# Kernel optimization log

Hardware: AMD Instinct MI355X
Metric: run time of the kernel (lower is better)

The kernel has to match this reference:

```python
import jax, jax.numpy as jnp
import numpy as np

EPS = 1e-6
SEARCH_RANGE = 4  # K = 2*R+1 = 9


def setup_inputs() -> dict:
    key = jax.random.key(0)
    k1, k2, k3, k4 = jax.random.split(key, 4)
    B, C, H, W = 4, 128, 128, 240
    E = 64
    F_L = jax.random.normal(k1, (B, C, H, W), dtype=jnp.float32)
    F_R = jax.random.normal(k2, (B, C, H, W), dtype=jnp.float32)
    d0 = jax.random.uniform(k3, (B, 1, H, W), dtype=jnp.float32) * 64.0  # pixel disparity
    phi_w = jax.random.normal(k4, (E, C), dtype=jnp.float32) / np.sqrt(C)  # 1x1 conv weight
    return {"F_L": F_L, "F_R": F_R, "d0": d0, "phi_w": phi_w}


def _embed(x, phi_w):
    # 1x1 conv + channel L2 normalize (cosine embedding)
    y = jnp.einsum('ec,bchw->behw', phi_w, x)
    norm = jnp.sqrt(jnp.sum(y * y, axis=1, keepdims=True)) + EPS
    return y / norm


def reference(F_L, F_R, d0, phi_w):
    R = SEARCH_RANGE
    FL = _embed(F_L, phi_w)  # (B,E,H,W)
    FR = _embed(F_R, phi_w)
    B, E, H, W = FL.shape
    deltas = jnp.arange(-R, R + 1, dtype=FL.dtype)  # (K,)
    xx = jnp.arange(W, dtype=FL.dtype)  # base x grid
    # x' = x - (d0 + delta); align_corners=True grid round-trips to pixel coords exactly,
    # y coordinate is identity, so warp is 1D bilinear along W with border clamp.
    xprime = xx[None, None, None, :] - d0[:, None, 0, :, :] - deltas[None, :, None, None]  # (B,K,H,W)
    x0 = jnp.floor(xprime)
    w = xprime - x0  # bilinear weight
    i0 = jnp.clip(x0.astype(jnp.int32), 0, W - 1)
    i1 = jnp.clip(x0.astype(jnp.int32) + 1, 0, W - 1)
    FR_e = FR[:, None]  # (B,1,E,H,W)
    g0 = jnp.take_along_axis(FR_e, i0[:, :, None, :, :], axis=4)  # (B,K,E,H,W)
    g1 = jnp.take_along_axis(FR_e, i1[:, :, None, :, :], axis=4)
    FR_s = g0 * (1.0 - w)[:, :, None] + g1 * w[:, :, None]
    cost_vol = jnp.einsum('behw,bkehw->bkhw', FL, FR_s)  # (B,K,H,W)
    return cost_vol
```

## Files before the change

### kernel.cpp

```cpp
#include <hip/hip_runtime.h>
#include <hip/hip_bf16.h>

#define NB 4
#define NC 128
#define NH 128
#define NW 240
#define NE 64
#define NK 9
#define PLANE (NH*NW)
#define CHW (NC*PLANE)
#define XS 244

typedef __attribute__((ext_vector_type(8))) short short8;
typedef __attribute__((ext_vector_type(4))) float f32x4;
typedef __attribute__((ext_vector_type(2))) __fp16 fp16x2;
typedef __attribute__((ext_vector_type(8))) __fp16 fp16x8;

__device__ __forceinline__ unsigned pkh(float x, float y){
  fp16x2 h = __builtin_amdgcn_cvt_pkrtz(x, y);
  return __builtin_bit_cast(unsigned, h);
}
__device__ __forceinline__ float fdot2u(unsigned a, unsigned b, float c){
#if __has_builtin(__builtin_amdgcn_fdot2)
  return __builtin_amdgcn_fdot2(__builtin_bit_cast(fp16x2,a),
                                __builtin_bit_cast(fp16x2,b), c, false);
#else
  fp16x2 ha = __builtin_bit_cast(fp16x2,a), hb = __builtin_bit_cast(fp16x2,b);
  return c + (float)ha[0]*(float)hb[0] + (float)ha[1]*(float)hb[1];
#endif
}
__device__ __forceinline__ int swz(int r){ return (r ^ (r>>3)) & 7; }

__global__ __launch_bounds__(1024, 8)
void fused_kernel(const float* __restrict__ xL,
                  const float* __restrict__ xR,
                  const float* __restrict__ d0g,
                  const float* __restrict__ phig,
                  float* __restrict__ outg)
{
  __shared__ __attribute__((aligned(16))) unsigned short xs[64*XS];
  __shared__ __attribute__((aligned(16))) unsigned short phis[NE*136];
  __shared__ __attribute__((aligned(16))) unsigned short FLb[NW*64];

  const int tid  = threadIdx.x;
  const int lane = tid & 63;
  const int wv   = tid >> 6;
  const int b    = blockIdx.x >> 7;
  const int h    = blockIdx.x & 127;
  const size_t base = (size_t)b*CHW + (size_t)h*NW;
  const int pixbase = (b*NH + h)*NW;

  const int mrow = lane & 15;
  const int kg   = lane >> 4;
  const int nt   = wv;
  const int n    = 16*nt + mrow;

  float d0v = (tid < 960) ? d0g[pixbase + (tid >> 2)] : 0.f;

  auto load_chunk = [&](const float* __restrict__ xg, int ch, float4 (&r)[4]) {
    if (tid < 960) {
      #pragma unroll
      for (int i = 0; i < 4; ++i) {
        unsigned idx = i*960 + tid;
        unsigned c = idx / 60u, s = idx - 60u*c;
        r[i] = *(const float4*)(xg + base + (size_t)(64*ch + c)*PLANE + 4*s);
      }
    }
  };
  auto write_chunk = [&](float4 (&r)[4]) {
    if (tid < 960) {
      #pragma unroll
      for (int i = 0; i < 4; ++i) {
        unsigned idx = i*960 + tid;
        unsigned c = idx / 60u, s = idx - 60u*c;
        uint2 pk; pk.x = pkh(r[i].x, r[i].y); pk.y = pkh(r[i].z, r[i].w);
        *(uint2*)&xs[c*XS + 4*s] = pk;
      }
    }
  };
  auto gemm_chunk = [&](f32x4 (&acc)[4], int ch) {
    if (nt < 15) {
      #pragma unroll
      for (int ks = 0; ks < 2; ++ks) {
        const int r0 = 32*ks + 8*kg;
        fp16x8 bv;
        #pragma unroll
        for (int j = 0; j < 8; ++j)
          bv[j] = *(const __fp16*)&xs[(r0 + j)*XS + n];
        #pragma unroll
        for (int mt = 0; mt < 4; ++mt) {
          short8 raw = *(const short8*)&phis[(16*mt + mrow)*136 + 64*ch + 32*ks + 8*kg];
          fp16x8 af = __builtin_bit_cast(fp16x8, raw);
          acc[mt] = __builtin_amdgcn_mfma_f32_16x16x32_f16(af, bv, acc[mt], 0, 0, 0);
        }
      }
    }
  };
  auto norm_pack = [&](f32x4 (&acc)[4], uint2 (&pk)[4]) {
    float ss = 0.f;
    #pragma unroll
    for (int mt = 0; mt < 4; ++mt)
      #pragma unroll
      for (int r = 0; r < 4; ++r)
        ss += acc[mt][r]*acc[mt][r];
    ss += __shfl_xor(ss, 16, 64);
    ss += __shfl_xor(ss, 32, 64);
    float inv = 1.f/(sqrtf(ss) + 1e-6f);
    #pragma unroll
    for (int mt = 0; mt < 4; ++mt) {
      pk[mt].x = pkh(acc[mt][0]*inv, acc[mt][1]*inv);
      pk[mt].y = pkh(acc[mt][2]*inv, acc[mt][3]*inv);
    }
  };

  float4 st[4];
  load_chunk(xL, 0, st);
  float4 pr[2];
  #pragma unroll
  for (int i = 0; i < 2; ++i) {
    int idx = i*1024 + tid;
    pr[i] = *(const float4*)(phig + (idx>>5)*128 + 4*(idx&31));
  }
  #pragma unroll
  for (int i = 0; i < 2; ++i) {
    int idx = i*1024 + tid;
    uint2 pk; pk.x = pkh(pr[i].x, pr[i].y); pk.y = pkh(pr[i].z, pr[i].w);
    *(uint2*)&phis[(idx>>5)*136 + 4*(idx&31)] = pk;
  }
  write_chunk(st);
  __syncthreads();

  f32x4 accL[4];
  #pragma unroll
  for (int mt = 0; mt < 4; ++mt) accL[mt] = (f32x4){0.f,0.f,0.f,0.f};

  load_chunk(xL, 1, st);
  gemm_chunk(accL, 0);
  __syncthreads();
  write_chunk(st);
  __syncthreads();

  load_chunk(xR, 0, st);
  gemm_chunk(accL, 1);
  uint2 flpk[4];
  norm_pack(accL, flpk);
  if (nt < 15) {
    #pragma unroll
    for (int mt = 0; mt < 4; ++mt) {
      int e0 = 16*mt + 4*kg;
      int pos = n*64 + (((e0>>3) ^ swz(n))<<3) + (e0&7);
      *(uint2*)&FLb[pos] = flpk[mt];
    }
  }
  __syncthreads();
  write_chunk(st);
  __syncthreads();

  f32x4 accR[4];
  #pragma unroll
  for (int mt = 0; mt < 4; ++mt) accR[mt] = (f32x4){0.f,0.f,0.f,0.f};

  load_chunk(xR, 1, st);
  gemm_chunk(accR, 0);
  __syncthreads();
  write_chunk(st);
  __syncthreads();

  gemm_chunk(accR, 1);
  uint2 frpk[4];
  norm_pack(accR, frpk);
  __syncthreads();

  unsigned short* FRb = &xs[0];
  if (nt < 15) {
    #pragma unroll
    for (int mt = 0; mt < 4; ++mt) {
      int e0 = 16*mt + 4*kg;
      int pos = n*64 + (((e0>>3) ^ swz(n))<<3) + (e0&7);
      *(uint2*)&FRb[pos] = frpk[mt];
    }
  }
  __syncthreads();

  float* cvb = (float*)phis;
  if (tid < 960) {
    const int p  = tid >> 2;
    const int eh = tid & 3;
    float xf  = (float)p - d0v;
    float x0  = floorf(xf);
    float wfr = xf - x0;
    int jb = (int)x0 - 4;

    unsigned fl[8];
    #pragma unroll
    for (int i = 0; i < 2; ++i) {
      int c4 = 2*eh + i;
      uint4 raw = *(const uint4*)&FLb[p*64 + ((c4 ^ swz(p))<<3)];
      fl[4*i+0]=raw.x; fl[4*i+1]=raw.y; fl[4*i+2]=raw.z; fl[4*i+3]=raw.w;
    }

    float D[10];
    #pragma unroll
    for (int t = 0; t < 10; ++t) {
      int j = jb + t;
      j = j < 0 ? 0 : (j > NW-1 ? NW-1 : j);
      float s = 0.f;
      #pragma unroll
      for (int i = 0; i < 2; ++i) {
        int c4 = 2*eh + i;
        uint4 raw = *(const uint4*)&FRb[j*64 + ((c4 ^ swz(j))<<3)];
        s = fdot2u(fl[4*i+0], raw.x, s);
        s = fdot2u(fl[4*i+1], raw.y, s);
        s = fdot2u(fl[4*i+2], raw.z, s);
        s = fdot2u(fl[4*i+3], raw.w, s);
      }
      D[t] = s;
    }
    #pragma unroll
    for (int t = 0; t < 10; ++t) {
      D[t] += __shfl_xor(D[t], 1, 64);
      D[t] += __shfl_xor(D[t], 2, 64);
    }

    #define WK(k) { const int t0 = 8-(k); cvb[(k)*NW + p] = (1.f - wfr)*D[t0] + wfr*D[t0+1]; }
    if      (eh == 0) { WK(0) WK(1) WK(2) }
    else if (eh == 1) { WK(3) WK(4) }
    else if (eh == 2) { WK(5) WK(6) }
    else              { WK(7) WK(8) }
    #undef WK
  }
  __syncthreads();

  if (tid < 540) {
    int k = tid/60, w4 = tid - 60*k;
    float4 v = *(const float4*)&cvb[k*NW + 4*w4];
    *(float4*)(outg + (size_t)b*NK*PLANE + (size_t)h*NW + (size_t)k*PLANE + 4*w4) = v;
  }
}

extern "C" void kernel_launch(void* const* d_in, const int* in_sizes, int n_in,
                              void* d_out, int out_size, void* d_ws, size_t ws_size,
                              hipStream_t stream) {
  const float* xL   = (const float*)d_in[0];
  const float* xR   = (const float*)d_in[1];
  const float* d0g  = (const float*)d_in[2];
  const float* phig = (const float*)d_in[3];
  float* outg = (float*)d_out;
  fused_kernel<<<dim3(NB*NH), dim3(1024), 0, stream>>>(xL, xR, d0g, phig, outg);
}
```

Baseline: 148.1 us.

## Stream input chunks directly to LDS with double-buffered global_load_lds pipeline

Replaces register-staged loads, fp16 conversion and LDS writes with direct global-to-LDS async loads (global_load_lds) into two fp32 LDS buffers of 32 channels each. Chunk loads are issued one stage ahead of the MFMA GEMM rounds, so memory traffic overlaps with compute. The fp16 conversion moves into the GEMM operand fetch. The separate FL buffer is dropped and the staging buffers are reused for the embeddings. This adds per-read conversions and relies on __syncthreads waiting for the outstanding LDS-direct loads.

```diff
diff --git a/kernel.cpp b/kernel.cpp
--- a/kernel.cpp
+++ b/kernel.cpp
@@ -9,7 +9,6 @@
 #define NK 9
 #define PLANE (NH*NW)
 #define CHW (NC*PLANE)
-#define XS 244
 
 typedef __attribute__((ext_vector_type(8))) short short8;
 typedef __attribute__((ext_vector_type(4))) float f32x4;
@@ -31,6 +30,16 @@
 }
 __device__ __forceinline__ int swz(int r){ return (r ^ (r>>3)) & 7; }
 
+__device__ __forceinline__ void gload_lds16(const float* g, float* lds_u, int lane){
+#if __has_builtin(__builtin_amdgcn_global_load_lds)
+  __builtin_amdgcn_global_load_lds(
+      (const __attribute__((address_space(1))) unsigned*)g,
+      (__attribute__((address_space(3))) unsigned*)lds_u, 16, 0, 0);
+#else
+  *(float4*)(lds_u + 4*lane) = *(const float4*)g;
+#endif
+}
+
 __global__ __launch_bounds__(1024, 8)
 void fused_kernel(const float* __restrict__ xL,
                   const float* __restrict__ xR,
@@ -38,9 +47,9 @@
                   const float* __restrict__ phig,
                   float* __restrict__ outg)
 {
-  __shared__ __attribute__((aligned(16))) unsigned short xs[64*XS];
+  __shared__ __attribute__((aligned(16))) float xs0[7680];
+  __shared__ __attribute__((aligned(16))) float xs1[7680];
   __shared__ __attribute__((aligned(16))) unsigned short phis[NE*136];
-  __shared__ __attribute__((aligned(16))) unsigned short FLb[NW*64];
 
   const int tid  = threadIdx.x;
   const int lane = tid & 63;
@@ -55,48 +64,38 @@
   const int nt   = wv;
   const int n    = 16*nt + mrow;
 
-  float d0v = (tid < 960) ? d0g[pixbase + (tid >> 2)] : 0.f;
-
-  auto load_chunk = [&](const float* __restrict__ xg, int ch, float4 (&r)[4]) {
-    if (tid < 960) {
-      #pragma unroll
-      for (int i = 0; i < 4; ++i) {
-        unsigned idx = i*960 + tid;
-        unsigned c = idx / 60u, s = idx - 60u*c;
-        r[i] = *(const float4*)(xg + base + (size_t)(64*ch + c)*PLANE + 4*s);
+  auto issue_chunk = [&](int q){
+    const float* src = (q < 4) ? xL : xR;
+    const int cb = 32*(q & 3);
+    float* buf = (q & 1) ? xs1 : xs0;
+    #pragma unroll
+    for (int i = 0; i < 2; ++i) {
+      int qq = 2*wv + i;
+      if (qq < 30) {
+        int g4 = qq*64 + lane;
+        int c = g4/60, s4 = g4 - 60*c;
+        gload_lds16(src + base + (size_t)(cb + c)*PLANE + 4*s4,
+                    buf + qq*256, lane);
       }
     }
   };
-  auto write_chunk = [&](float4 (&r)[4]) {
-    if (tid < 960) {
-      #pragma unroll
-      for (int i = 0; i < 4; ++i) {
-        unsigned idx = i*960 + tid;
-        unsigned c = idx / 60u, s = idx - 60u*c;
-        uint2 pk; pk.x = pkh(r[i].x, r[i].y); pk.y = pkh(r[i].z, r[i].w);
-        *(uint2*)&xs[c*XS + 4*s] = pk;
+
+  auto gemm_round = [&](const float* bf, int cb, f32x4 (&acc)[4]){
+    if (nt < 15) {
+      fp16x8 bv;
+      #pragma unroll
+      for (int j = 0; j < 8; ++j)
+        bv[j] = (__fp16)bf[(8*kg + j)*240 + n];
+      #pragma unroll
+      for (int mt = 0; mt < 4; ++mt) {
+        short8 raw = *(const short8*)&phis[(16*mt + mrow)*136 + cb + 8*kg];
+        fp16x8 af = __builtin_bit_cast(fp16x8, raw);
+        acc[mt] = __builtin_amdgcn_mfma_f32_16x16x32_f16(af, bv, acc[mt], 0, 0, 0);
       }
     }
   };
-  auto gemm_chunk = [&](f32x4 (&acc)[4], int ch) {
-    if (nt < 15) {
-      #pragma unroll
-      for (int ks = 0; ks < 2; ++ks) {
-        const int r0 = 32*ks + 8*kg;
-        fp16x8 bv;
-        #pragma unroll
-        for (int j = 0; j < 8; ++j)
-          bv[j] = *(const __fp16*)&xs[(r0 + j)*XS + n];
-        #pragma unroll
-        for (int mt = 0; mt < 4; ++mt) {
-          short8 raw = *(const short8*)&phis[(16*mt + mrow)*136 + 64*ch + 32*ks + 8*kg];
-          fp16x8 af = __builtin_bit_cast(fp16x8, raw);
-          acc[mt] = __builtin_amdgcn_mfma_f32_16x16x32_f16(af, bv, acc[mt], 0, 0, 0);
-        }
-      }
-    }
-  };
-  auto norm_pack = [&](f32x4 (&acc)[4], uint2 (&pk)[4]) {
+
+  auto norm_pack = [&](f32x4 (&acc)[4], uint2 (&pk)[4]){
     float ss = 0.f;
     #pragma unroll
     for (int mt = 0; mt < 4; ++mt)
@@ -113,8 +112,17 @@
     }
   };
 
-  float4 st[4];
-  load_chunk(xL, 0, st);
+  auto frag_write = [&](unsigned short* dst, uint2 (&pk)[4]){
+    #pragma unroll
+    for (int mt = 0; mt < 4; ++mt) {
+      int e0 = 16*mt + 4*kg;
+      int pos = n*64 + (((e0>>3) ^ swz(n))<<3) + (e0&7);
+      *(uint2*)&dst[pos] = pk[mt];
+    }
+  };
+
+  issue_chunk(0);
+  float d0v = (tid < 960) ? d0g[pixbase + (tid >> 2)] : 0.f;
   float4 pr[2];
   #pragma unroll
   for (int i = 0; i < 2; ++i) {
@@ -127,59 +135,31 @@
     uint2 pk; pk.x = pkh(pr[i].x, pr[i].y); pk.y = pkh(pr[i].z, pr[i].w);
     *(uint2*)&phis[(idx>>5)*136 + 4*(idx&31)] = pk;
   }
-  write_chunk(st);
-  __syncthreads();
-
-  f32x4 accL[4];
+
+  f32x4 accL[4], accR[4];
   #pragma unroll
-  for (int mt = 0; mt < 4; ++mt) accL[mt] = (f32x4){0.f,0.f,0.f,0.f};
-
-  load_chunk(xL, 1, st);
-  gemm_chunk(accL, 0);
-  __syncthreads();
-  write_chunk(st);
-  __syncthreads();
-
-  load_chunk(xR, 0, st);
-  gemm_chunk(accL, 1);
-  uint2 flpk[4];
-  norm_pack(accL, flpk);
-  if (nt < 15) {
-    #pragma unroll
-    for (int mt = 0; mt < 4; ++mt) {
-      int e0 = 16*mt + 4*kg;
-      int pos = n*64 + (((e0>>3) ^ swz(n))<<3) + (e0&7);
-      *(uint2*)&FLb[pos] = flpk[mt];
-    }
-  }
-  __syncthreads();
-  write_chunk(st);
-  __syncthreads();
-
-  f32x4 accR[4];
-  #pragma unroll
-  for (int mt = 0; mt < 4; ++mt) accR[mt] = (f32x4){0.f,0.f,0.f,0.f};
-
-  load_chunk(xR, 1, st);
-  gemm_chunk(accR, 0);
-  __syncthreads();
-  write_chunk(st);
-  __syncthreads();
-
-  gemm_chunk(accR, 1);
-  uint2 frpk[4];
-  norm_pack(accR, frpk);
-  __syncthreads();
-
-  unsigned short* FRb = &xs[0];
-  if (nt < 15) {
-    #pragma unroll
-    for (int mt = 0; mt < 4; ++mt) {
-      int e0 = 16*mt + 4*kg;
-      int pos = n*64 + (((e0>>3) ^ swz(n))<<3) + (e0&7);
-      *(uint2*)&FRb[pos] = frpk[mt];
-    }
-  }
+  for (int mt = 0; mt < 4; ++mt) {
+    accL[mt] = (f32x4){0.f,0.f,0.f,0.f};
+    accR[mt] = (f32x4){0.f,0.f,0.f,0.f};
+  }
+  uint2 flpk[4], frpk[4];
+
+  __syncthreads();  issue_chunk(1);  gemm_round(xs0,  0, accL);
+  __syncthreads();  issue_chunk(2);  gemm_round(xs1, 32, accL);
+  __syncthreads();  issue_chunk(3);  gemm_round(xs0, 64, accL);
+  __syncthreads();  issue_chunk(4);  gemm_round(xs1, 96, accL);
+  if (nt < 15) norm_pack(accL, flpk);
+  __syncthreads();  issue_chunk(5);  gemm_round(xs0,  0, accR);
+  __syncthreads();  issue_chunk(6);  gemm_round(xs1, 32, accR);
+  __syncthreads();  issue_chunk(7);  gemm_round(xs0, 64, accR);
+  __syncthreads();
+  unsigned short* FLb = (unsigned short*)xs0;
+  if (nt < 15) frag_write(FLb, flpk);
+  gemm_round(xs1, 96, accR);
+  if (nt < 15) norm_pack(accR, frpk);
+  __syncthreads();
+  unsigned short* FRb = (unsigned short*)xs1;
+  if (nt < 15) frag_write(FRb, frpk);
   __syncthreads();
 
   float* cvb = (float*)phis;
```

Result: no change. 149.8 us (+1.2%).
